# Performance work log

Measured on AMD Instinct MI355X. Metric: run time of the kernel, lower is better.

The kernel has to match this reference:

```python
import jax, jax.numpy as jnp
import numpy as np

IN_CH, OUT_CH, K, POOL = 3, 16, 3, 2

def setup_inputs() -> dict:
    key = jax.random.key(0)
    kx, kw, kb = jax.random.split(key, 3)
    B, H, W = 64, 512, 512
    x = jax.random.normal(kx, (B, IN_CH, H, W), dtype=jnp.float32)
    fan_in = IN_CH * K * K
    bound = 1.0 / np.sqrt(fan_in)
    weight = jax.random.uniform(kw, (OUT_CH, IN_CH, K, K), dtype=jnp.float32, minval=-bound, maxval=bound)
    bias = jax.random.uniform(kb, (OUT_CH,), dtype=jnp.float32, minval=-bound, maxval=bound)
    return {"x": x, "weight": weight, "bias": bias}

def reference(x, weight, bias):
    # Conv2d, stride 1, VALID padding (matches in_h - k + 1 in kernel)
    y = jax.lax.conv_general_dilated(
        x, weight, window_strides=(1, 1), padding="VALID",
        dimension_numbers=("NCHW", "OIHW", "NCHW"))
    y = y + bias[None, :, None, None]  # [B, OC, Hc, Wc]
    B, C, Hc, Wc = y.shape
    Hp, Wp = Hc // POOL, Wc // POOL
    # Average pool 2x2 (floor-cropped like the CUDA kernel's integer division)
    y = y[:, :, :Hp * POOL, :Wp * POOL].reshape(B, C, Hp, POOL, Wp, POOL).mean(axis=(3, 5))
    # Sigmoid then sum over channel + spatial dims -> one scalar per batch element
    return jax.nn.sigmoid(y).sum(axis=(1, 2, 3))
```

## Files before the change

kernel.cpp:

```cpp
#include <hip/hip_runtime.h>


#define IC 3
#define OCH 16
#define HH 512
#define WW 512
#define HP 255
#define SROWS 5
#define STRIPS 51

typedef float v2f __attribute__((ext_vector_type(2)));

__device__ __forceinline__ float fast_sigmoid(float v) {
    float e = __expf(-v);
    return __builtin_amdgcn_rcpf(1.0f + e);
}

__global__ void build_weff(const float* __restrict__ w,
                           const float* __restrict__ bias,
                           float* __restrict__ ws)
{
    const int i = threadIdx.x;
    for (int idx = i; idx < OCH * 48; idx += 256) {
        int oc = idx / 48;
        int rem = idx - oc * 48;
        int ic = rem >> 4;
        int ky = (rem >> 2) & 3;
        int kx = rem & 3;
        float s = 0.f;
#pragma unroll
        for (int py = 0; py < 2; ++py) {
            int r = ky - py;
            if (r < 0 || r > 2) continue;
#pragma unroll
            for (int px = 0; px < 2; ++px) {
                int c = kx - px;
                if (c < 0 || c > 2) continue;
                s += w[((oc * IC + ic) * 3 + r) * 3 + c];
            }
        }
        ws[oc * 64 + rem] = 0.25f * s;
    }
    if (i < OCH) ws[i * 64 + 48] = bias[i];
}

__global__ __launch_bounds__(128)
void conv_pool_sig_sum(const float* __restrict__ x,
                       const float* __restrict__ wws,
                       float* __restrict__ out)
{
    const int tid = threadIdx.x;
    const bool v1 = (tid < 127);
    const int c0 = 4 * tid;
    const int b = blockIdx.y;
    const int hp0 = blockIdx.x * SROWS;
    const int tail = v1 ? 4 : 0;

    const float* xb = x + ((size_t)b * IC * HH + (size_t)2 * hp0) * WW + c0;

    float lsum = 0.f, lsum1 = 0.f;

    for (int s = 0; s < SROWS; ++s) {
        float4 xa[IC][4];
        float2 xt[IC][4];
#pragma unroll
        for (int ic = 0; ic < IC; ++ic) {
            const float* pr = xb + (size_t)ic * HH * WW;
#pragma unroll
            for (int r = 0; r < 4; ++r) {
                xa[ic][r] = *(const float4*)(pr + r * WW);
                xt[ic][r] = *(const float2*)(pr + r * WW + tail);
            }
        }

#pragma unroll 1
        for (int oc = 0; oc < OCH; ++oc) {
            const float* we = wws + oc * 64;
            const float bv = we[48];
            v2f acc = {bv, bv};
#pragma unroll
            for (int ic = 0; ic < IC; ++ic) {
#pragma unroll
                for (int r = 0; r < 4; ++r) {
                    const float4 a = xa[ic][r];
                    const float2 t = xt[ic][r];
                    const float* wr = we + ic * 16 + r * 4;
                    acc += (v2f){a.x, a.z} * wr[0];
                    acc += (v2f){a.y, a.w} * wr[1];
                    acc += (v2f){a.z, t.x} * wr[2];
                    acc += (v2f){a.w, t.y} * wr[3];
                }
            }
            lsum  += fast_sigmoid(acc.x);
            lsum1 += fast_sigmoid(acc.y);
        }
        xb += 2 * WW;
    }
    lsum += v1 ? lsum1 : 0.f;

#pragma unroll
    for (int off = 32; off > 0; off >>= 1)
        lsum += __shfl_xor(lsum, off, 64);
    if ((tid & 63) == 0) atomicAdd(out + b, lsum);
}

extern "C" void kernel_launch(void* const* d_in, const int* in_sizes, int n_in,
                              void* d_out, int out_size, void* d_ws, size_t ws_size,
                              hipStream_t stream) {
    const float* x = (const float*)d_in[0];
    const float* w = (const float*)d_in[1];
    const float* bias = (const float*)d_in[2];
    float* out = (float*)d_out;
    float* wws = (float*)d_ws;

    hipMemsetAsync(out, 0, out_size * sizeof(float), stream);
    build_weff<<<1, 256, 0, stream>>>(w, bias, wws);

    dim3 grid(STRIPS, 64);
    conv_pool_sig_sum<<<grid, 128, 0, stream>>>(x, wws, out);
}
```

Before: 335.4 us.

## Reorder effective weights icr-major and fully unroll channel loop with 32 accumulators

Reorders the precomputed pooled-conv weight table so each input row's weights for all 16 output channels are contiguous, and rewrites the inner loop to sweep input rows outermost, keeping 32 scalar accumulators (two pooled outputs times 16 channels) instead of looping output channels with a v2f accumulator. The full unroll turns weight reads into scalar loads with fixed offsets and is meant to expose more independent FMAs. It also sets launch bounds to a minimum of 4 blocks per CU. The risks are higher register pressure, and the switch from packed v2f math to scalar FMAs may lose the packed-FMA throughput.

After: 472.8 us. +41.0%, slower.

```diff
diff --git a/kernel.cpp b/kernel.cpp
--- a/kernel.cpp
+++ b/kernel.cpp
@@ -9,8 +9,6 @@
 #define SROWS 5
 #define STRIPS 51
 
-typedef float v2f __attribute__((ext_vector_type(2)));
-
 __device__ __forceinline__ float fast_sigmoid(float v) {
     float e = __expf(-v);
     return __builtin_amdgcn_rcpf(1.0f + e);
@@ -21,12 +19,12 @@
                            float* __restrict__ ws)
 {
     const int i = threadIdx.x;
-    for (int idx = i; idx < OCH * 48; idx += 256) {
-        int oc = idx / 48;
-        int rem = idx - oc * 48;
-        int ic = rem >> 4;
-        int ky = (rem >> 2) & 3;
-        int kx = rem & 3;
+    for (int idx = i; idx < IC * 4 * OCH * 4; idx += 256) {
+        int kx = idx & 3;
+        int oc = (idx >> 2) & 15;
+        int icr = idx >> 6;
+        int ic = icr >> 2;
+        int ky = icr & 3;
         float s = 0.f;
 #pragma unroll
         for (int py = 0; py < 2; ++py) {
@@ -39,12 +37,12 @@
                 s += w[((oc * IC + ic) * 3 + r) * 3 + c];
             }
         }
-        ws[oc * 64 + rem] = 0.25f * s;
+        ws[idx] = 0.25f * s;
     }
-    if (i < OCH) ws[i * 64 + 48] = bias[i];
+    if (i < OCH) ws[IC * 4 * OCH * 4 + i] = bias[i];
 }
 
-__global__ __launch_bounds__(128)
+__global__ __launch_bounds__(128, 4)
 void conv_pool_sig_sum(const float* __restrict__ x,
                        const float* __restrict__ wws,
                        float* __restrict__ out)
@@ -57,9 +55,11 @@
     const int tail = v1 ? 4 : 0;
 
     const float* xb = x + ((size_t)b * IC * HH + (size_t)2 * hp0) * WW + c0;
+    const float* bp = wws + IC * 4 * OCH * 4;
 
-    float lsum = 0.f, lsum1 = 0.f;
+    float lsA = 0.f, lsB = 0.f;
 
+#pragma unroll 1
     for (int s = 0; s < SROWS; ++s) {
         float4 xa[IC][4];
         float2 xt[IC][4];
@@ -73,35 +73,38 @@
             }
         }
 
-#pragma unroll 1
+        float accA[OCH], accB[OCH];
+#pragma unroll
+        for (int oc = 0; oc < OCH; ++oc) { accA[oc] = bp[oc]; accB[oc] = bp[oc]; }
+
+#pragma unroll
+        for (int icr = 0; icr < IC * 4; ++icr) {
+            const int ic = icr >> 2, r = icr & 3;
+            const float4 a = xa[ic][r];
+            const float2 t = xt[ic][r];
+            const float* wp = wws + icr * 64;
+#pragma unroll
+            for (int oc = 0; oc < OCH; ++oc) {
+                const float w0 = wp[4 * oc + 0], w1 = wp[4 * oc + 1];
+                const float w2 = wp[4 * oc + 2], w3 = wp[4 * oc + 3];
+                accA[oc] += a.x * w0 + a.y * w1 + a.z * w2 + a.w * w3;
+                accB[oc] += a.z * w0 + a.w * w1 + t.x * w2 + t.y * w3;
+            }
+        }
+
+#pragma unroll
         for (int oc = 0; oc < OCH; ++oc) {
-            const float* we = wws + oc * 64;
-            const float bv = we[48];
-            v2f acc = {bv, bv};
-#pragma unroll
-            for (int ic = 0; ic < IC; ++ic) {
-#pragma unroll
-                for (int r = 0; r < 4; ++r) {
-                    const float4 a = xa[ic][r];
-                    const float2 t = xt[ic][r];
-                    const float* wr = we + ic * 16 + r * 4;
-                    acc += (v2f){a.x, a.z} * wr[0];
-                    acc += (v2f){a.y, a.w} * wr[1];
-                    acc += (v2f){a.z, t.x} * wr[2];
-                    acc += (v2f){a.w, t.y} * wr[3];
-                }
-            }
-            lsum  += fast_sigmoid(acc.x);
-            lsum1 += fast_sigmoid(acc.y);
+            lsA += fast_sigmoid(accA[oc]);
+            lsB += fast_sigmoid(accB[oc]);
         }
         xb += 2 * WW;
     }
-    lsum += v1 ? lsum1 : 0.f;
+    lsA += v1 ? lsB : 0.f;
 
 #pragma unroll
     for (int off = 32; off > 0; off >>= 1)
-        lsum += __shfl_xor(lsum, off, 64);
-    if ((tid & 63) == 0) atomicAdd(out + b, lsum);
+        lsA += __shfl_xor(lsA, off, 64);
+    if ((tid & 63) == 0) atomicAdd(out + b, lsA);
 }
 
 extern "C" void kernel_launch(void* const* d_in, const int* in_sizes, int n_in,
```

## Use one pooled row per block and pair output channels with packed weight FMAs

Applied to the files above, without the earlier changes.

Each block now handles a single pooled row instead of a strip of five, so the grid grows from 51 to 255 blocks per batch element and there are more waves in flight to hide memory latency. The inner loop handles two output channels per iteration. It splits the dot product across the two lanes of a packed float2 and loads weights as float2 vectors, so each packed FMA multiplies adjacent inputs by adjacent weights instead of broadcasting one weight. In exchange the kernel launches many more blocks, does more atomics and reductions per block, and adds one lane-sum per channel before the sigmoid.

Measured after the change: 512.1 us. 1.53x slower.

```diff
diff --git a/kernel.cpp b/kernel.cpp
--- a/kernel.cpp
+++ b/kernel.cpp
@@ -5,9 +5,6 @@
 #define OCH 16
 #define HH 512
 #define WW 512
-#define HP 255
-#define SROWS 5
-#define STRIPS 51
 
 typedef float v2f __attribute__((ext_vector_type(2)));
 
@@ -53,55 +50,62 @@
     const bool v1 = (tid < 127);
     const int c0 = 4 * tid;
     const int b = blockIdx.y;
-    const int hp0 = blockIdx.x * SROWS;
+    const int hp = blockIdx.x;
     const int tail = v1 ? 4 : 0;
 
-    const float* xb = x + ((size_t)b * IC * HH + (size_t)2 * hp0) * WW + c0;
+    const float* xb = x + ((size_t)b * IC * HH + (size_t)2 * hp) * WW + c0;
 
-    float lsum = 0.f, lsum1 = 0.f;
+    float4 xa[IC][4];
+    float2 xt[IC][4];
+#pragma unroll
+    for (int ic = 0; ic < IC; ++ic) {
+        const float* pr = xb + (size_t)ic * HH * WW;
+#pragma unroll
+        for (int r = 0; r < 4; ++r) {
+            xa[ic][r] = *(const float4*)(pr + r * WW);
+            xt[ic][r] = *(const float2*)(pr + r * WW + tail);
+        }
+    }
 
-    for (int s = 0; s < SROWS; ++s) {
-        float4 xa[IC][4];
-        float2 xt[IC][4];
+    float lsA = 0.f, lsB = 0.f;
+
+#pragma unroll 1
+    for (int ocp = 0; ocp < OCH / 2; ++ocp) {
+        const float* w0 = wws + (2 * ocp + 0) * 64;
+        const float* w1 = wws + (2 * ocp + 1) * 64;
+
+        v2f aA0 = {w0[48], 0.f}, aB0 = {w0[48], 0.f};
+        v2f aA1 = {w1[48], 0.f}, aB1 = {w1[48], 0.f};
+
 #pragma unroll
-        for (int ic = 0; ic < IC; ++ic) {
-            const float* pr = xb + (size_t)ic * HH * WW;
-#pragma unroll
-            for (int r = 0; r < 4; ++r) {
-                xa[ic][r] = *(const float4*)(pr + r * WW);
-                xt[ic][r] = *(const float2*)(pr + r * WW + tail);
-            }
+        for (int icr = 0; icr < IC * 4; ++icr) {
+            const int ic = icr >> 2, r = icr & 3;
+            const float4 a = xa[ic][r];
+            const float2 t = xt[ic][r];
+            const v2f xp01 = {a.x, a.y};
+            const v2f xp23 = {a.z, a.w};
+            const v2f xp45 = {t.x, t.y};
+            const v2f wa01 = *(const v2f*)(w0 + icr * 4);
+            const v2f wa23 = *(const v2f*)(w0 + icr * 4 + 2);
+            const v2f wb01 = *(const v2f*)(w1 + icr * 4);
+            const v2f wb23 = *(const v2f*)(w1 + icr * 4 + 2);
+            aA0 += xp01 * wa01;  aA0 += xp23 * wa23;
+            aB0 += xp23 * wa01;  aB0 += xp45 * wa23;
+            aA1 += xp01 * wb01;  aA1 += xp23 * wb23;
+            aB1 += xp23 * wb01;  aB1 += xp45 * wb23;
         }
 
-#pragma unroll 1
-        for (int oc = 0; oc < OCH; ++oc) {
-            const float* we = wws + oc * 64;
-            const float bv = we[48];
-            v2f acc = {bv, bv};
-#pragma unroll
-            for (int ic = 0; ic < IC; ++ic) {
-#pragma unroll
-                for (int r = 0; r < 4; ++r) {
-                    const float4 a = xa[ic][r];
-                    const float2 t = xt[ic][r];
-                    const float* wr = we + ic * 16 + r * 4;
-                    acc += (v2f){a.x, a.z} * wr[0];
-                    acc += (v2f){a.y, a.w} * wr[1];
-                    acc += (v2f){a.z, t.x} * wr[2];
-                    acc += (v2f){a.w, t.y} * wr[3];
-                }
-            }
-            lsum  += fast_sigmoid(acc.x);
-            lsum1 += fast_sigmoid(acc.y);
-        }
-        xb += 2 * WW;
+        lsA += fast_sigmoid(aA0.x + aA0.y);
+        lsB += fast_sigmoid(aB0.x + aB0.y);
+        lsA += fast_sigmoid(aA1.x + aA1.y);
+        lsB += fast_sigmoid(aB1.x + aB1.y);
     }
-    lsum += v1 ? lsum1 : 0.f;
+    lsA += v1 ? lsB : 0.f;
 
 #pragma unroll
     for (int off = 32; off > 0; off >>= 1)
-        lsum += __shfl_xor(lsum, off, 64);
-    if ((tid & 63) == 0) atomicAdd(out + b, lsum);
+        lsA += __shfl_xor(lsA, off, 64);
+    if ((tid & 63) == 0) atomicAdd(out + b, lsA);
 }
 
 extern "C" void kernel_launch(void* const* d_in, const int* in_sizes, int n_in,
@@ -116,6 +120,6 @@
     hipMemsetAsync(out, 0, out_size * sizeof(float), stream);
     build_weff<<<1, 256, 0, stream>>>(w, bias, wws);
 
-    dim3 grid(STRIPS, 64);
+    dim3 grid(255, 64);
     conv_pool_sig_sum<<<grid, 128, 0, stream>>>(x, wws, out);
 }
```
